# Performance work log

Measured on AMD Instinct MI355X. Metric: run time of the kernel, lower is better.

Reference implementation:

```python
import jax, jax.numpy as jnp
import numpy as np


def setup_inputs() -> dict:
    key = jax.random.key(0)
    kK, kV, kQ = jax.random.split(key, 3)
    B, D, S = 4, 64, 4096
    K = jax.random.normal(kK, (B, D, S), dtype=jnp.float32)
    V = jax.random.normal(kV, (B, D, S), dtype=jnp.float32)
    Q = jax.random.normal(kQ, (B, D, S), dtype=jnp.float32)
    return {"K": K, "V": V, "Q": Q}


def reference(K, V, Q):
    # K,V: [B, D, Sk], Q: [B, D, Sq]
    d = Q.shape[1]
    # A[b,k,q] = sum_d K[b,d,k] * Q[b,d,q] / sqrt(d)
    A = jnp.einsum("bdk,bdq->bkq", K, Q) / jnp.sqrt(jnp.asarray(d, Q.dtype))
    A = jax.nn.softmax(A, axis=1)  # normalize over keys (dim 1), matching F.softmax(A, 1)
    # R[b,d,q] = sum_k V[b,d,k] * A[b,k,q]
    R = jnp.einsum("bdk,bkq->bdq", V, A)
    return jnp.concatenate((R, Q), axis=1)  # [B, 2D, Sq]
```

## Files before the change

kernel.cpp:

```cpp
#include <hip/hip_runtime.h>
#include <hip/hip_bf16.h>

#define S_LEN 4096
#define D_DIM 64
#define QB 128
#define KB 64
#define NKB (S_LEN / KB)
#define WAVES 8

typedef __attribute__((ext_vector_type(8))) short bf16x8;
typedef __attribute__((ext_vector_type(4))) float f32x4;
typedef unsigned int u32;

union bpack8 { __hip_bfloat16 h[8]; bf16x8 v; };
union bpack4 { __hip_bfloat16 h[4]; uint2 v; };

static __device__ __forceinline__ float fexp2(float x) {
    return __builtin_amdgcn_exp2f(x);
}

#define GLD16(gp, lp) __builtin_amdgcn_global_load_lds( \
    (const __attribute__((address_space(1))) u32*)(const void*)(gp), \
    (__attribute__((address_space(3))) u32*)(void*)(lp), 16, 0, 0)

#define QSCALE 0.18033688011112042f

__global__ __launch_bounds__(256)
void prep_all(const float* __restrict__ K, const float* __restrict__ V,
              const float* __restrict__ Q,
              __hip_bfloat16* __restrict__ Kbf, __hip_bfloat16* __restrict__ Vbf,
              __hip_bfloat16* __restrict__ Qbf, float* __restrict__ out)
{
    const int b = blockIdx.y, which = blockIdx.z;

    if (which == 2) {
        const int kb = blockIdx.x;
        __hip_bfloat16* tile = Vbf + ((size_t)(b * NKB + kb) * D_DIM) * KB;
        const float* src = V + (size_t)b * D_DIM * S_LEN + kb * KB;
        #pragma unroll
        for (int s0 = 0; s0 < 512; s0 += 256) {
            int s = s0 + threadIdx.x;
            int d = s >> 3, j = s & 7;
            const float* p = src + (size_t)d * S_LEN + j * 8;
            float4 a = *(const float4*)p, c = *(const float4*)(p + 4);
            bpack8 u;
            u.h[0] = __float2bfloat16(a.x); u.h[1] = __float2bfloat16(a.y);
            u.h[2] = __float2bfloat16(a.z); u.h[3] = __float2bfloat16(a.w);
            u.h[4] = __float2bfloat16(c.x); u.h[5] = __float2bfloat16(c.y);
            u.h[6] = __float2bfloat16(c.z); u.h[7] = __float2bfloat16(c.w);
            *(bf16x8*)&tile[d * KB + (j ^ (d & 7)) * 8] = u.v;
        }
        return;
    }

    const int t0 = blockIdx.x * 64;
    const int lane = threadIdx.x & 63, wid = threadIdx.x >> 6;
    const float* in = which ? Q : K;
    const float* src = in + (size_t)b * D_DIM * S_LEN + t0;
    float r[16];
    #pragma unroll
    for (int j = 0; j < 16; ++j)
        r[j] = src[(size_t)(wid * 16 + j) * S_LEN + lane];

    if (which == 1) {
        float* o = out + ((size_t)b * 2 * D_DIM + D_DIM) * S_LEN + t0 + lane;
        #pragma unroll
        for (int j = 0; j < 16; ++j)
            o[(size_t)(wid * 16 + j) * S_LEN] = r[j];
    }

    const float sc = which ? QSCALE : 1.0f;
    __hip_bfloat16* ob = which ? Qbf : Kbf;
    __hip_bfloat16* dst = ob + ((size_t)b * S_LEN + t0 + lane) * D_DIM;
    #pragma unroll
    for (int h = 0; h < 2; ++h) {
        bpack8 u;
        #pragma unroll
        for (int e = 0; e < 8; ++e) u.h[e] = __float2bfloat16(r[h * 8 + e] * sc);
        int slot = (wid * 2 + h) ^ (lane & 7);
        *(bf16x8*)&dst[slot * 8] = u.v;
    }
}

__global__ __launch_bounds__(512, 6)
void attn_fwd(const __hip_bfloat16* __restrict__ Kbf,
              const __hip_bfloat16* __restrict__ Vbf,
              const __hip_bfloat16* __restrict__ Qbf,
              float* __restrict__ out,
              float* __restrict__ accP, float* __restrict__ lP,
              int base, int rem, int nb, int direct)
{
    const int b  = blockIdx.y;
    const int z  = blockIdx.z;
    const int q0 = blockIdx.x * QB;

    const int t    = threadIdx.x;
    const int lane = t & 63;
    const int wid  = t >> 6;
    const int lq   = lane & 15;
    const int kg   = lane >> 4;
    const int sx   = lq & 7;

    __shared__ __align__(16) __hip_bfloat16 Ks[2][KB * D_DIM];
    __shared__ __align__(16) __hip_bfloat16 Vs[2][KB * D_DIM];
    __shared__ __align__(16) __hip_bfloat16 Ps[WAVES][16][72];

    const __hip_bfloat16* qt    = Qbf + ((size_t)b * S_LEN + q0) * D_DIM;
    const __hip_bfloat16* kbase = Kbf + (size_t)b * S_LEN * D_DIM;
    const __hip_bfloat16* vbase = Vbf + (size_t)b * S_LEN * D_DIM;

    const int tile0  = z * base + (z < rem ? z : rem);
    const int ntiles = base + (z < rem ? 1 : 0);
    const int kstart = tile0 * KB;

    GLD16(qt + t * 8,        (char*)Ks + wid * 1024);
    GLD16(qt + 4096 + t * 8, (char*)Ks + 8192 + wid * 1024);
    __syncthreads();

    const __hip_bfloat16* Qs = (const __hip_bfloat16*)Ks;
    const int rq = wid * 16 + lq;
    const bf16x8 qf0 = *(const bf16x8*)&Qs[rq * 64 + ((kg ^ sx)) * 8];
    const bf16x8 qf1 = *(const bf16x8*)&Qs[rq * 64 + ((kg ^ sx) ^ 4) * 8];
    __syncthreads();

    GLD16(kbase + (size_t)kstart * D_DIM + t * 8, (char*)&Ks[0][0] + wid * 1024);
    GLD16(vbase + (size_t)kstart * D_DIM + t * 8, (char*)&Vs[0][0] + wid * 1024);
    __syncthreads();

    float lsum = 0.f;
    f32x4 acc[4] = {{0.f,0.f,0.f,0.f},{0.f,0.f,0.f,0.f},
                    {0.f,0.f,0.f,0.f},{0.f,0.f,0.f,0.f}};
    int cur = 0;

    for (int it = 0; it < ntiles; ++it) {
        if (it + 1 < ntiles) {
            const size_t ko = (size_t)(kstart + (it + 1) * KB) * D_DIM;
            GLD16(kbase + ko + t * 8, (char*)&Ks[cur ^ 1][0] + wid * 1024);
            GLD16(vbase + ko + t * 8, (char*)&Vs[cur ^ 1][0] + wid * 1024);
        }
        const __hip_bfloat16* Kc = &Ks[cur][0];
        const __hip_bfloat16* Vc = &Vs[cur][0];

        f32x4 s[4] = {{0.f,0.f,0.f,0.f},{0.f,0.f,0.f,0.f},
                      {0.f,0.f,0.f,0.f},{0.f,0.f,0.f,0.f}};
        __builtin_amdgcn_s_setprio(1);
        #pragma unroll
        for (int kt = 0; kt < 4; ++kt) {
            const int rk = kt * 16 + lq;
            bf16x8 af0 = *(const bf16x8*)&Kc[rk * 64 + ((kg ^ sx)) * 8];
            bf16x8 af1 = *(const bf16x8*)&Kc[rk * 64 + ((kg ^ sx) ^ 4) * 8];
            s[kt] = __builtin_amdgcn_mfma_f32_16x16x32_bf16(af0, qf0, s[kt], 0, 0, 0);
            s[kt] = __builtin_amdgcn_mfma_f32_16x16x32_bf16(af1, qf1, s[kt], 0, 0, 0);
        }
        __builtin_amdgcn_s_setprio(0);

        float ps = 0.f;
        #pragma unroll
        for (int kt = 0; kt < 4; ++kt) {
            bpack4 u;
            #pragma unroll
            for (int r = 0; r < 4; ++r) {
                float e = fexp2(s[kt][r]);
                ps += e;
                u.h[r] = __float2bfloat16(e);
            }
            *(uint2*)&Ps[wid][lq][kt * 16 + kg * 4] = u.v;
        }
        lsum += ps;
        asm volatile("" ::: "memory");

        bf16x8 pf0 = *(const bf16x8*)&Ps[wid][lq][kg * 8];
        bf16x8 pf1 = *(const bf16x8*)&Ps[wid][lq][32 + kg * 8];
        __builtin_amdgcn_s_setprio(1);
        #pragma unroll
        for (int dt = 0; dt < 4; ++dt) {
            const int rd = dt * 16 + lq;
            bf16x8 vf0 = *(const bf16x8*)&Vc[rd * 64 + ((kg ^ sx)) * 8];
            bf16x8 vf1 = *(const bf16x8*)&Vc[rd * 64 + ((kg ^ sx) ^ 4) * 8];
            acc[dt] = __builtin_amdgcn_mfma_f32_16x16x32_bf16(vf0, pf0, acc[dt], 0, 0, 0);
            acc[dt] = __builtin_amdgcn_mfma_f32_16x16x32_bf16(vf1, pf1, acc[dt], 0, 0, 0);
        }
        __builtin_amdgcn_s_setprio(0);

        __syncthreads();
        cur ^= 1;
    }

    lsum += __shfl_xor(lsum, 16);
    lsum += __shfl_xor(lsum, 32);

    const int qw = wid * 16;
    if (!direct) {
        size_t pb = ((size_t)z * nb + b) * D_DIM * S_LEN;
        #pragma unroll
        for (int dt = 0; dt < 4; ++dt)
            #pragma unroll
            for (int r = 0; r < 4; ++r) {
                int d = dt * 16 + kg * 4 + r;
                accP[pb + (size_t)d * S_LEN + q0 + qw + lq] = acc[dt][r];
            }
        if (kg == 0)
            lP[((size_t)z * nb + b) * S_LEN + q0 + qw + lq] = lsum;
    } else {
        float inv = 1.0f / lsum;
        const size_t ob = (size_t)b * (2 * D_DIM) * S_LEN;
        #pragma unroll
        for (int dt = 0; dt < 4; ++dt)
            #pragma unroll
            for (int r = 0; r < 4; ++r) {
                int d = dt * 16 + kg * 4 + r;
                out[ob + (size_t)d * S_LEN + q0 + qw + lq] = acc[dt][r] * inv;
            }
    }
}

__global__ __launch_bounds__(256)
void attn_combine(const float* __restrict__ accP, const float* __restrict__ lP,
                  float* __restrict__ out, int nsplit, int nb)
{
    int gid = blockIdx.x * 256 + threadIdx.x;
    int q4  = gid & (S_LEN / 4 - 1);
    int rest = gid >> 10;
    int d    = rest & (D_DIM - 1);
    int b    = rest >> 6;
    if (b >= nb) return;
    size_t qoff = (size_t)q4 * 4;

    float num[4] = {0.f,0.f,0.f,0.f}, den[4] = {0.f,0.f,0.f,0.f};
    for (int z = 0; z < nsplit; ++z) {
        float4 lz = *(const float4*)&lP[((size_t)z * nb + b) * S_LEN + qoff];
        float4 az = *(const float4*)&accP[(((size_t)z * nb + b) * D_DIM + d) * S_LEN + qoff];
        num[0] += az.x; num[1] += az.y; num[2] += az.z; num[3] += az.w;
        den[0] += lz.x; den[1] += lz.y; den[2] += lz.z; den[3] += lz.w;
    }
    float4 r;
    r.x = num[0] / den[0]; r.y = num[1] / den[1];
    r.z = num[2] / den[2]; r.w = num[3] / den[3];
    *(float4*)&out[((size_t)b * 2 * D_DIM + d) * S_LEN + qoff] = r;
}

extern "C" void kernel_launch(void* const* d_in, const int* in_sizes, int n_in,
                              void* d_out, int out_size, void* d_ws, size_t ws_size,
                              hipStream_t stream) {
    const float* K = (const float*)d_in[0];
    const float* V = (const float*)d_in[1];
    const float* Q = (const float*)d_in[2];
    float* out = (float*)d_out;

    const int B = in_sizes[0] / (D_DIM * S_LEN);
    const size_t bfE = (size_t)B * S_LEN * D_DIM;
    const size_t bf_bytes = 3 * bfE * sizeof(__hip_bfloat16);

    auto need = [&](int ns) -> size_t {
        return bf_bytes
             + (size_t)ns * B * D_DIM * S_LEN * 4
             + (size_t)ns * B * S_LEN * 4;
    };
    int nsplit = 6;
    if (need(nsplit) > ws_size) {
        nsplit = 4;
        while (nsplit > 1 && need(nsplit) > ws_size) nsplit >>= 1;
    }
    const int direct = (nsplit == 1);

    __hip_bfloat16* Kbf = (__hip_bfloat16*)d_ws;
    __hip_bfloat16* Vbf = Kbf + bfE;
    __hip_bfloat16* Qbf = Vbf + bfE;
    float* accP = (float*)(Qbf + bfE);
    float* lP   = accP + (size_t)nsplit * B * D_DIM * S_LEN;

    const int NT = S_LEN / KB;
    const int base = NT / nsplit, rem = NT % nsplit;

    dim3 pg(S_LEN / 64, B, 3);
    prep_all<<<pg, dim3(256), 0, stream>>>(K, V, Q, Kbf, Vbf, Qbf, out);

    dim3 grid(S_LEN / QB, B, nsplit);
    attn_fwd<<<grid, dim3(512), 0, stream>>>(Kbf, Vbf, Qbf, out, accP, lP,
                                             base, rem, B, direct);
    if (!direct) {
        int total = B * D_DIM * (S_LEN / 4);
        attn_combine<<<dim3(total / 256), dim3(256), 0, stream>>>(
            accP, lP, out, nsplit, B);
    }
}
```

Before: 41.01 us.

## Switch attention to 32x32 MFMA with register-resident P and bf16 partials

Rewrites the attention kernel to use 32x32x16 bf16 MFMA with 4 waves of 32 queries each and 32-key tiles. The softmax probabilities stay in registers, packed with cvt_pk and permlane32_swap instead of going through LDS. K and V are now interleaved into one per-tile buffer so each tile arrives in a single LDS region. Q is loaded directly from global memory, and the prep kernel is restructured. Partial accumulators are stored as bf16 with a larger split count (up to 10), which cuts combine traffic but loses some precision in the partial sums.

```diff
diff --git a/kernel.cpp b/kernel.cpp
--- a/kernel.cpp
+++ b/kernel.cpp
@@ -4,19 +4,30 @@
 #define S_LEN 4096
 #define D_DIM 64
 #define QB 128
-#define KB 64
-#define NKB (S_LEN / KB)
-#define WAVES 8
-
-typedef __attribute__((ext_vector_type(8))) short bf16x8;
-typedef __attribute__((ext_vector_type(4))) float f32x4;
+#define KB 32
+#define NT (S_LEN / KB)
+#define TILE_E 4096
+
+typedef __attribute__((ext_vector_type(8)))  short bf16x8;
+typedef __attribute__((ext_vector_type(16))) float f32x16;
 typedef unsigned int u32;
 
+#define Z16 {0.f,0.f,0.f,0.f,0.f,0.f,0.f,0.f,0.f,0.f,0.f,0.f,0.f,0.f,0.f,0.f}
+
 union bpack8 { __hip_bfloat16 h[8]; bf16x8 v; };
-union bpack4 { __hip_bfloat16 h[4]; uint2 v; };
+union ppack  { u32 w[4]; bf16x8 v; };
+union bload4 { uint2 u; __hip_bfloat16 h[4]; };
 
 static __device__ __forceinline__ float fexp2(float x) {
     return __builtin_amdgcn_exp2f(x);
+}
+static __device__ __forceinline__ u32 cvtpk(float lo, float hi) {
+    u32 r;
+    asm("v_cvt_pk_bf16_f32 %0, %1, %2" : "=v"(r) : "v"(lo), "v"(hi));
+    return r;
+}
+static __device__ __forceinline__ void plswap(u32 &a, u32 &b) {
+    asm("v_permlane32_swap_b32 %0, %1" : "+v"(a), "+v"(b));
 }
 
 #define GLD16(gp, lp) __builtin_amdgcn_global_load_lds( \
@@ -28,66 +39,51 @@
 __global__ __launch_bounds__(256)
 void prep_all(const float* __restrict__ K, const float* __restrict__ V,
               const float* __restrict__ Q,
-              __hip_bfloat16* __restrict__ Kbf, __hip_bfloat16* __restrict__ Vbf,
-              __hip_bfloat16* __restrict__ Qbf, float* __restrict__ out)
+              __hip_bfloat16* __restrict__ KVbf, __hip_bfloat16* __restrict__ Qbf,
+              float* __restrict__ out)
 {
-    const int b = blockIdx.y, which = blockIdx.z;
-
-    if (which == 2) {
-        const int kb = blockIdx.x;
-        __hip_bfloat16* tile = Vbf + ((size_t)(b * NKB + kb) * D_DIM) * KB;
-        const float* src = V + (size_t)b * D_DIM * S_LEN + kb * KB;
-        #pragma unroll
-        for (int s0 = 0; s0 < 512; s0 += 256) {
-            int s = s0 + threadIdx.x;
-            int d = s >> 3, j = s & 7;
-            const float* p = src + (size_t)d * S_LEN + j * 8;
-            float4 a = *(const float4*)p, c = *(const float4*)(p + 4);
-            bpack8 u;
-            u.h[0] = __float2bfloat16(a.x); u.h[1] = __float2bfloat16(a.y);
-            u.h[2] = __float2bfloat16(a.z); u.h[3] = __float2bfloat16(a.w);
-            u.h[4] = __float2bfloat16(c.x); u.h[5] = __float2bfloat16(c.y);
-            u.h[6] = __float2bfloat16(c.z); u.h[7] = __float2bfloat16(c.w);
-            *(bf16x8*)&tile[d * KB + (j ^ (d & 7)) * 8] = u.v;
-        }
-        return;
-    }
-
-    const int t0 = blockIdx.x * 64;
-    const int lane = threadIdx.x & 63, wid = threadIdx.x >> 6;
-    const float* in = which ? Q : K;
-    const float* src = in + (size_t)b * D_DIM * S_LEN + t0;
-    float r[16];
-    #pragma unroll
-    for (int j = 0; j < 16; ++j)
-        r[j] = src[(size_t)(wid * 16 + j) * S_LEN + lane];
-
-    if (which == 1) {
-        float* o = out + ((size_t)b * 2 * D_DIM + D_DIM) * S_LEN + t0 + lane;
-        #pragma unroll
-        for (int j = 0; j < 16; ++j)
-            o[(size_t)(wid * 16 + j) * S_LEN] = r[j];
-    }
-
-    const float sc = which ? QSCALE : 1.0f;
-    __hip_bfloat16* ob = which ? Qbf : Kbf;
-    __hip_bfloat16* dst = ob + ((size_t)b * S_LEN + t0 + lane) * D_DIM;
-    #pragma unroll
-    for (int h = 0; h < 2; ++h) {
+    const int b = blockIdx.y, x = blockIdx.x, z = blockIdx.z;
+    const int t = threadIdx.x;
+
+    if (z == 0) {
+        const int key = t & 31, dg = t >> 5;
+        const float* src = K + ((size_t)b * D_DIM + dg * 8) * S_LEN + x * KB + key;
         bpack8 u;
         #pragma unroll
-        for (int e = 0; e < 8; ++e) u.h[e] = __float2bfloat16(r[h * 8 + e] * sc);
-        int slot = (wid * 2 + h) ^ (lane & 7);
-        *(bf16x8*)&dst[slot * 8] = u.v;
-    }
-}
-
-__global__ __launch_bounds__(512, 6)
-void attn_fwd(const __hip_bfloat16* __restrict__ Kbf,
-              const __hip_bfloat16* __restrict__ Vbf,
+        for (int e = 0; e < 8; ++e)
+            u.h[e] = __float2bfloat16(src[(size_t)e * S_LEN]);
+        *(bf16x8*)&KVbf[((size_t)b * NT + x) * TILE_E + t * 8] = u.v;
+    } else if (z == 1) {
+        const int kg = t >> 6, d = t & 63;
+        const float* p = V + ((size_t)b * D_DIM + d) * S_LEN + x * KB + kg * 8;
+        float4 a = *(const float4*)p, c = *(const float4*)(p + 4);
+        bpack8 u;
+        u.h[0] = __float2bfloat16(a.x); u.h[1] = __float2bfloat16(a.y);
+        u.h[2] = __float2bfloat16(a.z); u.h[3] = __float2bfloat16(a.w);
+        u.h[4] = __float2bfloat16(c.x); u.h[5] = __float2bfloat16(c.y);
+        u.h[6] = __float2bfloat16(c.z); u.h[7] = __float2bfloat16(c.w);
+        *(bf16x8*)&KVbf[((size_t)b * NT + x) * TILE_E + 2048 + t * 8] = u.v;
+    } else {
+        const int q = x * 32 + (t & 31), dg = t >> 5;
+        const float* src = Q + ((size_t)b * D_DIM + dg * 8) * S_LEN + q;
+        float r[8];
+        #pragma unroll
+        for (int e = 0; e < 8; ++e) r[e] = src[(size_t)e * S_LEN];
+        float* o = out + ((size_t)b * 2 * D_DIM + D_DIM + dg * 8) * S_LEN + q;
+        #pragma unroll
+        for (int e = 0; e < 8; ++e) o[(size_t)e * S_LEN] = r[e];
+        bpack8 u;
+        #pragma unroll
+        for (int e = 0; e < 8; ++e) u.h[e] = __float2bfloat16(r[e] * QSCALE);
+        *(bf16x8*)&Qbf[((size_t)b * S_LEN + q) * D_DIM + dg * 8] = u.v;
+    }
+}
+
+__global__ __launch_bounds__(256, 5)
+void attn_fwd(const __hip_bfloat16* __restrict__ KVbf,
               const __hip_bfloat16* __restrict__ Qbf,
               float* __restrict__ out,
-              float* __restrict__ accP, float* __restrict__ lP,
+              __hip_bfloat16* __restrict__ accPb, float* __restrict__ lP,
               int base, int rem, int nb, int direct)
 {
     const int b  = blockIdx.y;
@@ -96,130 +92,113 @@
 
     const int t    = threadIdx.x;
     const int lane = t & 63;
-    const int wid  = t >> 6;
-    const int lq   = lane & 15;
-    const int kg   = lane >> 4;
-    const int sx   = lq & 7;
-
-    __shared__ __align__(16) __hip_bfloat16 Ks[2][KB * D_DIM];
-    __shared__ __align__(16) __hip_bfloat16 Vs[2][KB * D_DIM];
-    __shared__ __align__(16) __hip_bfloat16 Ps[WAVES][16][72];
-
-    const __hip_bfloat16* qt    = Qbf + ((size_t)b * S_LEN + q0) * D_DIM;
-    const __hip_bfloat16* kbase = Kbf + (size_t)b * S_LEN * D_DIM;
-    const __hip_bfloat16* vbase = Vbf + (size_t)b * S_LEN * D_DIM;
+    const int w    = t >> 6;
+    const int l5   = lane & 31;
+    const int h    = lane >> 5;
+
+    __shared__ __align__(16) char Ls[2][8192];
 
     const int tile0  = z * base + (z < rem ? z : rem);
     const int ntiles = base + (z < rem ? 1 : 0);
-    const int kstart = tile0 * KB;
-
-    GLD16(qt + t * 8,        (char*)Ks + wid * 1024);
-    GLD16(qt + 4096 + t * 8, (char*)Ks + 8192 + wid * 1024);
+    const __hip_bfloat16* kvb = KVbf + ((size_t)b * NT + tile0) * TILE_E;
+
+    const __hip_bfloat16* qrow = Qbf + ((size_t)b * S_LEN + q0 + w * 32 + l5) * D_DIM;
+    bf16x8 qf[4];
+    #pragma unroll
+    for (int j = 0; j < 4; ++j)
+        qf[j] = *(const bf16x8*)&qrow[(2 * j + h) * 8];
+
+    GLD16(kvb + w * 512 + lane * 8,        Ls[0] + w * 1024);
+    GLD16(kvb + 2048 + w * 512 + lane * 8, Ls[0] + 4096 + w * 1024);
     __syncthreads();
 
-    const __hip_bfloat16* Qs = (const __hip_bfloat16*)Ks;
-    const int rq = wid * 16 + lq;
-    const bf16x8 qf0 = *(const bf16x8*)&Qs[rq * 64 + ((kg ^ sx)) * 8];
-    const bf16x8 qf1 = *(const bf16x8*)&Qs[rq * 64 + ((kg ^ sx) ^ 4) * 8];
-    __syncthreads();
-
-    GLD16(kbase + (size_t)kstart * D_DIM + t * 8, (char*)&Ks[0][0] + wid * 1024);
-    GLD16(vbase + (size_t)kstart * D_DIM + t * 8, (char*)&Vs[0][0] + wid * 1024);
-    __syncthreads();
-
     float lsum = 0.f;
-    f32x4 acc[4] = {{0.f,0.f,0.f,0.f},{0.f,0.f,0.f,0.f},
-                    {0.f,0.f,0.f,0.f},{0.f,0.f,0.f,0.f}};
+    f32x16 acc[2] = {Z16, Z16};
     int cur = 0;
 
     for (int it = 0; it < ntiles; ++it) {
         if (it + 1 < ntiles) {
-            const size_t ko = (size_t)(kstart + (it + 1) * KB) * D_DIM;
-            GLD16(kbase + ko + t * 8, (char*)&Ks[cur ^ 1][0] + wid * 1024);
-            GLD16(vbase + ko + t * 8, (char*)&Vs[cur ^ 1][0] + wid * 1024);
+            const __hip_bfloat16* nx = kvb + (size_t)(it + 1) * TILE_E;
+            GLD16(nx + w * 512 + lane * 8,        Ls[cur ^ 1] + w * 1024);
+            GLD16(nx + 2048 + w * 512 + lane * 8, Ls[cur ^ 1] + 4096 + w * 1024);
         }
-        const __hip_bfloat16* Kc = &Ks[cur][0];
-        const __hip_bfloat16* Vc = &Vs[cur][0];
-
-        f32x4 s[4] = {{0.f,0.f,0.f,0.f},{0.f,0.f,0.f,0.f},
-                      {0.f,0.f,0.f,0.f},{0.f,0.f,0.f,0.f}};
+        const char* Lk = Ls[cur];
+        const char* Lv = Ls[cur] + 4096;
+
+        f32x16 s = Z16;
         __builtin_amdgcn_s_setprio(1);
         #pragma unroll
-        for (int kt = 0; kt < 4; ++kt) {
-            const int rk = kt * 16 + lq;
-            bf16x8 af0 = *(const bf16x8*)&Kc[rk * 64 + ((kg ^ sx)) * 8];
-            bf16x8 af1 = *(const bf16x8*)&Kc[rk * 64 + ((kg ^ sx) ^ 4) * 8];
-            s[kt] = __builtin_amdgcn_mfma_f32_16x16x32_bf16(af0, qf0, s[kt], 0, 0, 0);
-            s[kt] = __builtin_amdgcn_mfma_f32_16x16x32_bf16(af1, qf1, s[kt], 0, 0, 0);
+        for (int j = 0; j < 4; ++j) {
+            bf16x8 kf = *(const bf16x8*)(Lk + ((2 * j + h) * 32 + l5) * 16);
+            s = __builtin_amdgcn_mfma_f32_32x32x16_bf16(kf, qf[j], s, 0, 0, 0);
         }
         __builtin_amdgcn_s_setprio(0);
 
+        float e[16];
+        #pragma unroll
+        for (int r = 0; r < 16; ++r) e[r] = fexp2(s[r]);
         float ps = 0.f;
         #pragma unroll
-        for (int kt = 0; kt < 4; ++kt) {
-            bpack4 u;
+        for (int r = 0; r < 16; ++r) ps += e[r];
+        lsum += ps;
+
+        u32 A = cvtpk(e[0],  e[1]),  Bw = cvtpk(e[2],  e[3]);
+        u32 C = cvtpk(e[4],  e[5]),  Dw = cvtpk(e[6],  e[7]);
+        u32 E = cvtpk(e[8],  e[9]),  F  = cvtpk(e[10], e[11]);
+        u32 G = cvtpk(e[12], e[13]), H  = cvtpk(e[14], e[15]);
+        plswap(A, C); plswap(Bw, Dw); plswap(E, G); plswap(F, H);
+        ppack pf[2];
+        pf[0].w[0] = A; pf[0].w[1] = Bw; pf[0].w[2] = C; pf[0].w[3] = Dw;
+        pf[1].w[0] = E; pf[1].w[1] = F;  pf[1].w[2] = G; pf[1].w[3] = H;
+
+        __builtin_amdgcn_s_setprio(1);
+        #pragma unroll
+        for (int j = 0; j < 2; ++j)
             #pragma unroll
-            for (int r = 0; r < 4; ++r) {
-                float e = fexp2(s[kt][r]);
-                ps += e;
-                u.h[r] = __float2bfloat16(e);
+            for (int dt = 0; dt < 2; ++dt) {
+                bf16x8 vf = *(const bf16x8*)(Lv + ((2 * j + h) * 64 + dt * 32 + l5) * 16);
+                acc[dt] = __builtin_amdgcn_mfma_f32_32x32x16_bf16(vf, pf[j].v, acc[dt], 0, 0, 0);
             }
-            *(uint2*)&Ps[wid][lq][kt * 16 + kg * 4] = u.v;
-        }
-        lsum += ps;
-        asm volatile("" ::: "memory");
-
-        bf16x8 pf0 = *(const bf16x8*)&Ps[wid][lq][kg * 8];
-        bf16x8 pf1 = *(const bf16x8*)&Ps[wid][lq][32 + kg * 8];
-        __builtin_amdgcn_s_setprio(1);
-        #pragma unroll
-        for (int dt = 0; dt < 4; ++dt) {
-            const int rd = dt * 16 + lq;
-            bf16x8 vf0 = *(const bf16x8*)&Vc[rd * 64 + ((kg ^ sx)) * 8];
-            bf16x8 vf1 = *(const bf16x8*)&Vc[rd * 64 + ((kg ^ sx) ^ 4) * 8];
-            acc[dt] = __builtin_amdgcn_mfma_f32_16x16x32_bf16(vf0, pf0, acc[dt], 0, 0, 0);
-            acc[dt] = __builtin_amdgcn_mfma_f32_16x16x32_bf16(vf1, pf1, acc[dt], 0, 0, 0);
-        }
         __builtin_amdgcn_s_setprio(0);
 
         __syncthreads();
         cur ^= 1;
     }
 
-    lsum += __shfl_xor(lsum, 16);
     lsum += __shfl_xor(lsum, 32);
 
-    const int qw = wid * 16;
+    const int qcol = q0 + w * 32 + l5;
     if (!direct) {
-        size_t pb = ((size_t)z * nb + b) * D_DIM * S_LEN;
-        #pragma unroll
-        for (int dt = 0; dt < 4; ++dt)
+        __hip_bfloat16* ap = accPb + (size_t)(z * nb + b) * D_DIM * S_LEN;
+        #pragma unroll
+        for (int dt = 0; dt < 2; ++dt)
             #pragma unroll
-            for (int r = 0; r < 4; ++r) {
-                int d = dt * 16 + kg * 4 + r;
-                accP[pb + (size_t)d * S_LEN + q0 + qw + lq] = acc[dt][r];
+            for (int r = 0; r < 16; ++r) {
+                int d = dt * 32 + (r & 3) + 8 * (r >> 2) + 4 * h;
+                ap[(size_t)d * S_LEN + qcol] = __float2bfloat16(acc[dt][r]);
             }
-        if (kg == 0)
-            lP[((size_t)z * nb + b) * S_LEN + q0 + qw + lq] = lsum;
+        if (h == 0)
+            lP[(size_t)(z * nb + b) * S_LEN + qcol] = lsum;
     } else {
-        float inv = 1.0f / lsum;
-        const size_t ob = (size_t)b * (2 * D_DIM) * S_LEN;
-        #pragma unroll
-        for (int dt = 0; dt < 4; ++dt)
+        float inv = 1.f / lsum;
+        float* op = out + (size_t)b * 2 * D_DIM * S_LEN;
+        #pragma unroll
+        for (int dt = 0; dt < 2; ++dt)
             #pragma unroll
-            for (int r = 0; r < 4; ++r) {
-                int d = dt * 16 + kg * 4 + r;
-                out[ob + (size_t)d * S_LEN + q0 + qw + lq] = acc[dt][r] * inv;
+            for (int r = 0; r < 16; ++r) {
+                int d = dt * 32 + (r & 3) + 8 * (r >> 2) + 4 * h;
+                op[(size_t)d * S_LEN + qcol] = acc[dt][r] * inv;
             }
     }
 }
 
 __global__ __launch_bounds__(256)
-void attn_combine(const float* __restrict__ accP, const float* __restrict__ lP,
+void attn_combine(const __hip_bfloat16* __restrict__ accPb,
+                  const float* __restrict__ lP,
                   float* __restrict__ out, int nsplit, int nb)
 {
     int gid = blockIdx.x * 256 + threadIdx.x;
-    int q4  = gid & (S_LEN / 4 - 1);
+    int q4   = gid & (S_LEN / 4 - 1);
     int rest = gid >> 10;
     int d    = rest & (D_DIM - 1);
     int b    = rest >> 6;
@@ -228,9 +207,11 @@
 
     float num[4] = {0.f,0.f,0.f,0.f}, den[4] = {0.f,0.f,0.f,0.f};
     for (int z = 0; z < nsplit; ++z) {
-        float4 lz = *(const float4*)&lP[((size_t)z * nb + b) * S_LEN + qoff];
-        float4 az = *(const float4*)&accP[(((size_t)z * nb + b) * D_DIM + d) * S_LEN + qoff];
-        num[0] += az.x; num[1] += az.y; num[2] += az.z; num[3] += az.w;
+        bload4 a;
+        a.u = *(const uint2*)&accPb[((size_t)(z * nb + b) * D_DIM + d) * S_LEN + qoff];
+        float4 lz = *(const float4*)&lP[(size_t)(z * nb + b) * S_LEN + qoff];
+        num[0] += __bfloat162float(a.h[0]); num[1] += __bfloat162float(a.h[1]);
+        num[2] += __bfloat162float(a.h[2]); num[3] += __bfloat162float(a.h[3]);
         den[0] += lz.x; den[1] += lz.y; den[2] += lz.z; den[3] += lz.w;
     }
     float4 r;
@@ -248,39 +229,35 @@
     float* out = (float*)d_out;
 
     const int B = in_sizes[0] / (D_DIM * S_LEN);
-    const size_t bfE = (size_t)B * S_LEN * D_DIM;
-    const size_t bf_bytes = 3 * bfE * sizeof(__hip_bfloat16);
+    const size_t kvE = (size_t)B * NT * TILE_E;
+    const size_t qE  = (size_t)B * S_LEN * D_DIM;
 
     auto need = [&](int ns) -> size_t {
-        return bf_bytes
-             + (size_t)ns * B * D_DIM * S_LEN * 4
+        return (kvE + qE) * 2
+             + (size_t)ns * B * D_DIM * S_LEN * 2
              + (size_t)ns * B * S_LEN * 4;
     };
-    int nsplit = 6;
-    if (need(nsplit) > ws_size) {
-        nsplit = 4;
-        while (nsplit > 1 && need(nsplit) > ws_size) nsplit >>= 1;
-    }
+    const int cand[6] = {10, 8, 5, 4, 2, 1};
+    int nsplit = 1;
+    for (int i = 0; i < 6; ++i)
+        if (need(cand[i]) <= ws_size) { nsplit = cand[i]; break; }
     const int direct = (nsplit == 1);
 
-    __hip_bfloat16* Kbf = (__hip_bfloat16*)d_ws;
-    __hip_bfloat16* Vbf = Kbf + bfE;
-    __hip_bfloat16* Qbf = Vbf + bfE;
-    float* accP = (float*)(Qbf + bfE);
-    float* lP   = accP + (size_t)nsplit * B * D_DIM * S_LEN;
-
-    const int NT = S_LEN / KB;
+    __hip_bfloat16* KVbf = (__hip_bfloat16*)d_ws;
+    __hip_bfloat16* Qbf  = KVbf + kvE;
+    __hip_bfloat16* accPb = Qbf + qE;
+    float* lP = (float*)(accPb + (size_t)nsplit * B * D_DIM * S_LEN);
+
     const int base = NT / nsplit, rem = NT % nsplit;
 
-    dim3 pg(S_LEN / 64, B, 3);
-    prep_all<<<pg, dim3(256), 0, stream>>>(K, V, Q, Kbf, Vbf, Qbf, out);
-
-    dim3 grid(S_LEN / QB, B, nsplit);
-    attn_fwd<<<grid, dim3(512), 0, stream>>>(Kbf, Vbf, Qbf, out, accP, lP,
-                                             base, rem, B, direct);
+    prep_all<<<dim3(NT, B, 3), dim3(256), 0, stream>>>(K, V, Q, KVbf, Qbf, out);
+
+    attn_fwd<<<dim3(S_LEN / QB, B, nsplit), dim3(256), 0, stream>>>(
+        KVbf, Qbf, out, accPb, lP, base, rem, B, direct);
+
     if (!direct) {
         int total = B * D_DIM * (S_LEN / 4);
         attn_combine<<<dim3(total / 256), dim3(256), 0, stream>>>(
-            accP, lP, out, nsplit, B);
-    }
-}
+            accPb, lP, out, nsplit, B);
+    }
+}
```

After: 39.52 us. -3.6%, faster.
